# Kernel tuning notes

Hardware: AMD Instinct MI355X
Metric: run time of the kernel (lower is better)

## Reference

```python
import jax, jax.numpy as jnp
import numpy as np

B, S, D, F, V, R = 4, 1024, 768, 3072, 2048, 8


def setup_inputs() -> dict:
    key = jax.random.key(0)
    k_x, k_r, k_w1, k_b1, k_w2, k_b2 = jax.random.split(key, 6)
    e_two = jax.random.normal(k_x, (B, S, D), dtype=jnp.float32)
    route_ids = jax.random.randint(k_r, (B, S), 0, R, dtype=jnp.int32)
    # Per-route classification head params (stacked over route axis R).
    W1 = jax.random.normal(k_w1, (R, D, F), dtype=jnp.float32) / np.sqrt(D)
    b1 = jnp.zeros((R, F), dtype=jnp.float32)
    W2 = jax.random.normal(k_w2, (R, F, V), dtype=jnp.float32) / np.sqrt(F)
    b2 = jnp.zeros((R, V), dtype=jnp.float32)
    return {"e_two": e_two, "route_ids": route_ids,
            "W1": W1, "b1": b1, "W2": W2, "b2": b2}


def reference(e_two, route_ids, W1, b1, W2, b2):
    # Each token goes through the MLP classification head selected by its
    # route_id:  softmax(relu(x @ W1[r] + b1[r]) @ W2[r] + b2[r]).
    # Dense formulation: run every route head over all tokens (R is a small
    # fixed set), then gather each token's own route output.
    h = jax.nn.relu(jnp.einsum('bsd,rdf->rbsf', e_two, W1)
                    + b1[:, None, None, :])            # [R,B,S,F]
    logits_all = jnp.einsum('rbsf,rfv->rbsv', h, W2) + b2[:, None, None, :]
    # Select per-token route: [R,B,S,V] -> [B,S,R,V] -> gather along R.
    logits_all = jnp.moveaxis(logits_all, 0, 2)        # [B,S,R,V]
    idx = route_ids[:, :, None, None].astype(jnp.int32)  # [B,S,1,1]
    logits = jnp.take_along_axis(logits_all, idx, axis=2)[:, :, 0, :]  # [B,S,V]
    return jax.nn.softmax(logits, axis=-1)
```

## Files before the change

### kernel.cpp

```cpp
#include <hip/hip_runtime.h>


typedef __attribute__((ext_vector_type(8))) short    s16x8;
typedef __attribute__((ext_vector_type(4))) float    f32x4;

#define T_TOK 4096
#define D_    768
#define F_    3072
#define V_    2048
#define R_    8
#define BM    64
#define BN    128
#define BK    64
#define MAXTILES 72
#define PADROWS  4608

#define OFF_COUNTS  ((size_t)0)
#define OFF_CURS    ((size_t)64)
#define OFF_PADOFF  ((size_t)128)
#define OFF_NT      ((size_t)192)
#define OFF_TROUTE  ((size_t)256)
#define OFF_TROW    ((size_t)1024)
#define OFF_TOK     ((size_t)4096)
#define OFF_XG      ((size_t)32768)
#define OFF_H       (OFF_XG  + (size_t)PADROWS*D_*2)
#define OFF_W1T     (OFF_H   + (size_t)PADROWS*F_*2)
#define OFF_W2T     (OFF_W1T + (size_t)R_*F_*D_*2)

static __device__ __forceinline__ unsigned short f2bf(float f) {
  union { float f; unsigned int u; } x; x.f = f;
  unsigned int r = x.u + 0x7FFFu + ((x.u >> 16) & 1u);
  return (unsigned short)(r >> 16);
}

static __device__ __forceinline__ void gload_lds16(const unsigned short* g,
                                                   unsigned short* l) {
  __builtin_amdgcn_global_load_lds(
      (const __attribute__((address_space(1))) unsigned int*)(const void*)g,
      (__attribute__((address_space(3))) unsigned int*)(void*)l, 16, 0, 0);
}

__global__ void cr_count(const int* __restrict__ route, int* __restrict__ counts) {
  int t = blockIdx.x * blockDim.x + threadIdx.x;
  if (t < T_TOK) atomicAdd(&counts[route[t]], 1);
}

__global__ void cr_plan(const int* __restrict__ counts, int* __restrict__ padOff,
                        int* __restrict__ nTiles, int* __restrict__ tRoute,
                        int* __restrict__ tRow) {
  if (threadIdx.x != 0 || blockIdx.x != 0) return;
  int off = 0, tiles = 0;
  for (int r = 0; r < R_; ++r) {
    padOff[r] = off;
    int nt = (counts[r] + BM - 1) / BM;
    for (int i = 0; i < nt; ++i) { tRoute[tiles] = r; tRow[tiles] = off + i * BM; ++tiles; }
    off += nt * BM;
  }
  padOff[R_] = off;
  *nTiles = tiles;
}

__global__ void cr_scatter(const float* __restrict__ X, const int* __restrict__ route,
                           const int* __restrict__ padOff, int* __restrict__ curs,
                           int* __restrict__ tok, unsigned short* __restrict__ Xg) {
  __shared__ int spos;
  int t = blockIdx.x;
  if (threadIdx.x == 0) {
    int r = route[t];
    int p = padOff[r] + atomicAdd(&curs[r], 1);
    tok[p] = t;
    spos = p;
  }
  __syncthreads();
  int pos = spos;
  float4 v = reinterpret_cast<const float4*>(X + (size_t)t * D_)[threadIdx.x];
  ushort4 o;
  o.x = f2bf(v.x); o.y = f2bf(v.y); o.z = f2bf(v.z); o.w = f2bf(v.w);
  *reinterpret_cast<ushort4*>(Xg + (size_t)pos * D_ + threadIdx.x * 4) = o;
}

template <int K, int N>
__global__ void cr_transpose(const float* __restrict__ W, unsigned short* __restrict__ Wt) {
  __shared__ float tile[64][65];
  int r = blockIdx.z;
  const float* Wr = W + (size_t)r * K * N;
  unsigned short* Wtr = Wt + (size_t)r * N * K;
  int k0 = blockIdx.x * 64, n0 = blockIdx.y * 64;
  int t = threadIdx.x;
  int cb = (t & 15) * 4, rb = t >> 4;
#pragma unroll
  for (int i = 0; i < 4; ++i) {
    int k = rb + i * 16;
    float4 v = *reinterpret_cast<const float4*>(Wr + (size_t)(k0 + k) * N + n0 + cb);
    tile[k][cb] = v.x; tile[k][cb + 1] = v.y; tile[k][cb + 2] = v.z; tile[k][cb + 3] = v.w;
  }
  __syncthreads();
  int n = t >> 2, kc = (t & 3) * 16;
  alignas(16) unsigned short o[16];
#pragma unroll
  for (int j = 0; j < 16; ++j) o[j] = f2bf(tile[kc + j][n]);
  unsigned short* dst = Wtr + (size_t)(n0 + n) * K + k0 + kc;
  *reinterpret_cast<s16x8*>(dst)     = *reinterpret_cast<const s16x8*>(&o[0]);
  *reinterpret_cast<s16x8*>(dst + 8) = *reinterpret_cast<const s16x8*>(&o[8]);
}

template <int K, int N, int MODE>
__global__ __launch_bounds__(256) void cr_gemm(
    const unsigned short* __restrict__ A, const unsigned short* __restrict__ Wt,
    const float* __restrict__ bias, const int* __restrict__ nTiles,
    const int* __restrict__ tRoute, const int* __restrict__ tRow,
    const int* __restrict__ tok, unsigned short* __restrict__ Hout,
    float* __restrict__ Fout) {
  int mt = blockIdx.x;
  if (mt >= *nTiles) return;
  int route = tRoute[mt], row0 = tRow[mt];
  int col0 = blockIdx.y * BN;
  const unsigned short* Ag = A + (size_t)row0 * K;
  const unsigned short* Bg = Wt + ((size_t)route * N + col0) * K;

  __shared__ __align__(16) unsigned short As[BM * BK];
  __shared__ __align__(16) unsigned short Bs[BN * BK];

  int tid = threadIdx.x, lane = tid & 63, w = tid >> 6;
  int srow = lane >> 3;
  int scol = (lane & 7) * 8;
  int frow = lane & 15;
  int fk   = (lane >> 4) * 8;

  f32x4 acc[4][2] = {};

  for (int kt = 0; kt < K; kt += BK) {
#pragma unroll
    for (int j = 0; j < 6; ++j) {
      int chunk = j * 4 + w;
      if (chunk < 8) {
        int rrow = chunk * 8 + srow;
        gload_lds16(Ag + (size_t)rrow * K + kt + scol, As + chunk * 512);
      } else {
        int bcol = (chunk - 8) * 8 + srow;
        gload_lds16(Bg + (size_t)bcol * K + kt + scol, Bs + (chunk - 8) * 512);
      }
    }
    __syncthreads();
#pragma unroll
    for (int kk = 0; kk < 2; ++kk) {
      s16x8 a[4], b[2];
#pragma unroll
      for (int mi = 0; mi < 4; ++mi)
        a[mi] = *reinterpret_cast<const s16x8*>(&As[(mi * 16 + frow) * BK + kk * 32 + fk]);
#pragma unroll
      for (int ni = 0; ni < 2; ++ni)
        b[ni] = *reinterpret_cast<const s16x8*>(&Bs[(w * 32 + ni * 16 + frow) * BK + kk * 32 + fk]);
#pragma unroll
      for (int mi = 0; mi < 4; ++mi)
#pragma unroll
        for (int ni = 0; ni < 2; ++ni)
          acc[mi][ni] = __builtin_amdgcn_mfma_f32_16x16x32_bf16(a[mi], b[ni], acc[mi][ni], 0, 0, 0);
    }
    __syncthreads();
  }

  int crow = (lane >> 4) * 4;
  int ccol = lane & 15;
#pragma unroll
  for (int mi = 0; mi < 4; ++mi) {
#pragma unroll
    for (int ni = 0; ni < 2; ++ni) {
      int gcol = col0 + w * 32 + ni * 16 + ccol;
      float bv = bias[(size_t)route * N + gcol];
#pragma unroll
      for (int j = 0; j < 4; ++j) {
        int prow = row0 + mi * 16 + crow + j;
        float v = acc[mi][ni][j] + bv;
        if (MODE == 0) {
          v = fmaxf(v, 0.f);
          Hout[(size_t)prow * N + gcol] = f2bf(v);
        } else {
          int tk = tok[prow];
          if (tk >= 0) Fout[(size_t)tk * N + gcol] = v;
        }
      }
    }
  }
}

__global__ void cr_softmax(float* __restrict__ out) {
  int row = blockIdx.x;
  float* p = out + (size_t)row * V_;
  int t = threadIdx.x;
  float4 v0 = reinterpret_cast<float4*>(p)[t];
  float4 v1 = reinterpret_cast<float4*>(p)[t + 256];
  float m = fmaxf(fmaxf(fmaxf(v0.x, v0.y), fmaxf(v0.z, v0.w)),
                  fmaxf(fmaxf(v1.x, v1.y), fmaxf(v1.z, v1.w)));
#pragma unroll
  for (int o = 32; o; o >>= 1) m = fmaxf(m, __shfl_xor(m, o));
  __shared__ float sm[4], ss[4];
  int w = t >> 6;
  if ((t & 63) == 0) sm[w] = m;
  __syncthreads();
  m = fmaxf(fmaxf(sm[0], sm[1]), fmaxf(sm[2], sm[3]));
  v0.x = expf(v0.x - m); v0.y = expf(v0.y - m); v0.z = expf(v0.z - m); v0.w = expf(v0.w - m);
  v1.x = expf(v1.x - m); v1.y = expf(v1.y - m); v1.z = expf(v1.z - m); v1.w = expf(v1.w - m);
  float s = v0.x + v0.y + v0.z + v0.w + v1.x + v1.y + v1.z + v1.w;
#pragma unroll
  for (int o = 32; o; o >>= 1) s += __shfl_xor(s, o);
  if ((t & 63) == 0) ss[w] = s;
  __syncthreads();
  s = ss[0] + ss[1] + ss[2] + ss[3];
  float inv = 1.f / s;
  v0.x *= inv; v0.y *= inv; v0.z *= inv; v0.w *= inv;
  v1.x *= inv; v1.y *= inv; v1.z *= inv; v1.w *= inv;
  reinterpret_cast<float4*>(p)[t] = v0;
  reinterpret_cast<float4*>(p)[t + 256] = v1;
}

extern "C" void kernel_launch(void* const* d_in, const int* in_sizes, int n_in,
                              void* d_out, int out_size, void* d_ws, size_t ws_size,
                              hipStream_t stream) {
  const float* X      = (const float*)d_in[0];
  const int*   route  = (const int*)d_in[1];
  const float* W1     = (const float*)d_in[2];
  const float* b1     = (const float*)d_in[3];
  const float* W2     = (const float*)d_in[4];
  const float* b2     = (const float*)d_in[5];
  float*       out    = (float*)d_out;
  char*        ws     = (char*)d_ws;

  int* counts = (int*)(ws + OFF_COUNTS);
  int* curs   = (int*)(ws + OFF_CURS);
  int* padOff = (int*)(ws + OFF_PADOFF);
  int* nT     = (int*)(ws + OFF_NT);
  int* tRoute = (int*)(ws + OFF_TROUTE);
  int* tRow   = (int*)(ws + OFF_TROW);
  int* tok    = (int*)(ws + OFF_TOK);
  unsigned short* Xg  = (unsigned short*)(ws + OFF_XG);
  unsigned short* H   = (unsigned short*)(ws + OFF_H);
  unsigned short* W1T = (unsigned short*)(ws + OFF_W1T);
  unsigned short* W2T = (unsigned short*)(ws + OFF_W2T);

  hipMemsetAsync(ws, 0, 4096, stream);
  hipMemsetAsync(ws + OFF_TOK, 0xFF, (size_t)PADROWS * 4, stream);
  hipMemsetAsync(ws + OFF_XG, 0, (size_t)PADROWS * D_ * 2, stream);

  cr_count<<<T_TOK / 256, 256, 0, stream>>>(route, counts);
  cr_plan<<<1, 64, 0, stream>>>(counts, padOff, nT, tRoute, tRow);
  cr_scatter<<<T_TOK, 192, 0, stream>>>(X, route, padOff, curs, tok, Xg);

  cr_transpose<D_, F_><<<dim3(D_ / 64, F_ / 64, R_), 256, 0, stream>>>(W1, W1T);
  cr_transpose<F_, V_><<<dim3(F_ / 64, V_ / 64, R_), 256, 0, stream>>>(W2, W2T);

  cr_gemm<D_, F_, 0><<<dim3(MAXTILES, F_ / BN), 256, 0, stream>>>(
      Xg, W1T, b1, nT, tRoute, tRow, tok, H, nullptr);
  cr_gemm<F_, V_, 1><<<dim3(MAXTILES, V_ / BN), 256, 0, stream>>>(
      H, W2T, b2, nT, tRoute, tRow, tok, nullptr, out);

  cr_softmax<<<T_TOK, 256, 0, stream>>>(out);
}
```

Before: 652.0 us.

## Double-buffer LDS tiles in routed GEMM and remap blocks for XCD locality

The grouped GEMM now double-buffers its A and B shared-memory tiles. The next K-slice is issued with direct-to-LDS loads while MFMAs run on the current slice, which removes one barrier per iteration. The launch grid is flattened and block IDs are remapped so that all column blocks of an M-tile land on the same XCD (block index mod 8), which should improve L2 reuse of the activation rows. This doubles the LDS footprint, which may lower occupancy, and the overlap relies on the async LDS loads not being waited on before compute.

Result: no change. 646.4 us (-0.9%).

```diff
diff --git a/kernel.cpp b/kernel.cpp
--- a/kernel.cpp
+++ b/kernel.cpp
@@ -13,6 +13,7 @@
 #define BN    128
 #define BK    64
 #define MAXTILES 72
+#define NMTX     9
 #define PADROWS  4608
 
 #define OFF_COUNTS  ((size_t)0)
@@ -111,15 +112,20 @@
     const int* __restrict__ tRoute, const int* __restrict__ tRow,
     const int* __restrict__ tok, unsigned short* __restrict__ Hout,
     float* __restrict__ Fout) {
-  int mt = blockIdx.x;
+  int bid = blockIdx.x;
+  int xcd = bid & 7;
+  int widx = bid >> 3;
+  int mtl = widx % NMTX;
+  int y   = widx / NMTX;
+  int mt  = mtl * 8 + xcd;
   if (mt >= *nTiles) return;
   int route = tRoute[mt], row0 = tRow[mt];
-  int col0 = blockIdx.y * BN;
+  int col0 = y * BN;
   const unsigned short* Ag = A + (size_t)row0 * K;
   const unsigned short* Bg = Wt + ((size_t)route * N + col0) * K;
 
-  __shared__ __align__(16) unsigned short As[BM * BK];
-  __shared__ __align__(16) unsigned short Bs[BN * BK];
+  __shared__ __align__(16) unsigned short As[2][BM * BK];
+  __shared__ __align__(16) unsigned short Bs[2][BN * BK];
 
   int tid = threadIdx.x, lane = tid & 63, w = tid >> 6;
   int srow = lane >> 3;
@@ -129,36 +135,50 @@
 
   f32x4 acc[4][2] = {};
 
-  for (int kt = 0; kt < K; kt += BK) {
+  auto stage = [&](int buf, int kt) {
 #pragma unroll
     for (int j = 0; j < 6; ++j) {
       int chunk = j * 4 + w;
       if (chunk < 8) {
-        int rrow = chunk * 8 + srow;
-        gload_lds16(Ag + (size_t)rrow * K + kt + scol, As + chunk * 512);
+        gload_lds16(Ag + (size_t)(chunk * 8 + srow) * K + kt + scol,
+                    &As[buf][chunk * 512]);
       } else {
-        int bcol = (chunk - 8) * 8 + srow;
-        gload_lds16(Bg + (size_t)bcol * K + kt + scol, Bs + (chunk - 8) * 512);
+        gload_lds16(Bg + (size_t)((chunk - 8) * 8 + srow) * K + kt + scol,
+                    &Bs[buf][(chunk - 8) * 512]);
       }
     }
-    __syncthreads();
+  };
+  auto compute = [&](int buf) {
 #pragma unroll
     for (int kk = 0; kk < 2; ++kk) {
       s16x8 a[4], b[2];
 #pragma unroll
       for (int mi = 0; mi < 4; ++mi)
-        a[mi] = *reinterpret_cast<const s16x8*>(&As[(mi * 16 + frow) * BK + kk * 32 + fk]);
+        a[mi] = *reinterpret_cast<const s16x8*>(
+            &As[buf][(mi * 16 + frow) * BK + kk * 32 + fk]);
 #pragma unroll
       for (int ni = 0; ni < 2; ++ni)
-        b[ni] = *reinterpret_cast<const s16x8*>(&Bs[(w * 32 + ni * 16 + frow) * BK + kk * 32 + fk]);
+        b[ni] = *reinterpret_cast<const s16x8*>(
+            &Bs[buf][(w * 32 + ni * 16 + frow) * BK + kk * 32 + fk]);
 #pragma unroll
       for (int mi = 0; mi < 4; ++mi)
 #pragma unroll
         for (int ni = 0; ni < 2; ++ni)
-          acc[mi][ni] = __builtin_amdgcn_mfma_f32_16x16x32_bf16(a[mi], b[ni], acc[mi][ni], 0, 0, 0);
+          acc[mi][ni] = __builtin_amdgcn_mfma_f32_16x16x32_bf16(
+              a[mi], b[ni], acc[mi][ni], 0, 0, 0);
     }
+  };
+
+  stage(0, 0);
+  __syncthreads();
+  int cur = 0;
+  for (int kt = BK; kt < K; kt += BK) {
+    stage(cur ^ 1, kt);
+    compute(cur);
     __syncthreads();
-  }
+    cur ^= 1;
+  }
+  compute(cur);
 
   int crow = (lane >> 4) * 4;
   int ccol = lane & 15;
@@ -249,9 +269,9 @@
   cr_transpose<D_, F_><<<dim3(D_ / 64, F_ / 64, R_), 256, 0, stream>>>(W1, W1T);
   cr_transpose<F_, V_><<<dim3(F_ / 64, V_ / 64, R_), 256, 0, stream>>>(W2, W2T);
 
-  cr_gemm<D_, F_, 0><<<dim3(MAXTILES, F_ / BN), 256, 0, stream>>>(
+  cr_gemm<D_, F_, 0><<<MAXTILES * (F_ / BN), 256, 0, stream>>>(
       Xg, W1T, b1, nT, tRoute, tRow, tok, H, nullptr);
-  cr_gemm<F_, V_, 1><<<dim3(MAXTILES, V_ / BN), 256, 0, stream>>>(
+  cr_gemm<F_, V_, 1><<<MAXTILES * (V_ / BN), 256, 0, stream>>>(
       H, W2T, b2, nT, tRoute, tRow, tok, nullptr, out);
 
   cr_softmax<<<T_TOK, 256, 0, stream>>>(out);
```
